# Kernel tuning notes

Hardware: AMD Instinct MI355X
Metric: run time of the kernel (lower is better)

## Reference

```python
import jax, jax.numpy as jnp
import numpy as np

HID, D, NH, NL = 1024, 64, 16, 128  # hidden_dim, head_dim, num_head, num_landmarks


def iterative_inv(mat, n_iter=6):
    # Moore-Penrose pseudo-inverse via Newton-Schulz (Nystromformer), fp32.
    I = jnp.eye(mat.shape[-1], dtype=mat.dtype)
    K = mat
    denom = (jnp.max(jnp.sum(jnp.abs(K), axis=-2), axis=-1)
             * jnp.max(jnp.sum(jnp.abs(K), axis=-1), axis=-1))[..., None, None]
    V = jnp.swapaxes(K, -1, -2) / denom  # Z0 = K^T / (||K||_1 ||K||_inf)
    for _ in range(n_iter):
        KV = K @ V
        V = 0.25 * V @ (13.0 * I - KV @ (15.0 * I - KV @ (7.0 * I - KV)))
    return V


def nystrom_forward(X, mask, Wq, bq, Wk, bk, Wv, bv, Wo, bo):
    B, orig_len, _ = X.shape
    pad_len = NL - orig_len % NL  # always >= 1, matches torch code
    L = orig_len + pad_len
    Xp = jnp.pad(X, ((0, 0), (0, pad_len), (0, 0)))

    def split(Y):  # [B, L, NH*D] -> [B, NH, L, D]
        return Y.reshape(B, L, NH, D).transpose(0, 2, 1, 3)

    Q = split(Xp @ Wq.T + bq).astype(jnp.float32)
    K = split(Xp @ Wk.T + bk).astype(jnp.float32)
    V = split(Xp @ Wv.T + bv).astype(jnp.float32)

    m = mask[:, None, :, None]  # [B,1,L,1]
    scale = 1.0 / (D ** 0.25)   # 1/sqrt(sqrt(head_dim)) applied to both Q and K
    Q = Q * m * scale
    K = K * m * scale

    seg = L // NL
    Q_l = Q.reshape(B, NH, NL, seg, D).mean(axis=-2)  # landmarks via segment means
    K_l = K.reshape(B, NH, NL, seg, D).mean(axis=-2)

    kernel_1 = jax.nn.softmax(jnp.einsum('bhnd,bhld->bhnl', Q, K_l), axis=-1)   # [B,H,L,NL]
    kernel_2 = jax.nn.softmax(jnp.einsum('bhld,bhmd->bhlm', Q_l, K_l), axis=-1)  # [B,H,NL,NL]
    scores_3 = jnp.einsum('bhld,bhnd->bhln', Q_l, K) - 1e9 * (1.0 - mask[:, None, None, :])
    kernel_3 = jax.nn.softmax(scores_3, axis=-1)                                 # [B,H,NL,L]

    out = kernel_1 @ (iterative_inv(kernel_2) @ (kernel_3 @ V))  # [B,H,L,D]
    out = out.transpose(0, 2, 1, 3).reshape(B, L, NH * D)
    out = out @ Wo.T + bo
    return out[:, :orig_len]


def setup_inputs() -> dict:
    key = jax.random.key(0)
    ks = jax.random.split(key, 9)
    B, S = 2, 4095
    Lpad = S + (NL - S % NL)
    s = 0.02
    return {
        'X': jax.random.normal(ks[0], (B, S, HID), dtype=jnp.float32),
        'mask': jnp.ones((B, Lpad), dtype=jnp.float32),
        'Wq': jax.random.normal(ks[1], (NH * D, HID), dtype=jnp.float32) * s,
        'bq': jnp.zeros((NH * D,), dtype=jnp.float32),
        'Wk': jax.random.normal(ks[2], (NH * D, HID), dtype=jnp.float32) * s,
        'bk': jnp.zeros((NH * D,), dtype=jnp.float32),
        'Wv': jax.random.normal(ks[3], (NH * D, HID), dtype=jnp.float32) * s,
        'bv': jnp.zeros((NH * D,), dtype=jnp.float32),
        'Wo': jax.random.normal(ks[4], (HID, NH * D), dtype=jnp.float32) * s,
        'bo': jnp.zeros((HID,), dtype=jnp.float32),
    }


def reference(X, mask, Wq, bq, Wk, bk, Wv, bv, Wo, bo):
    return nystrom_forward(X, mask, Wq, bq, Wk, bk, Wv, bv, Wo, bo)
```

## Files before the change

### kernel.cpp

```cpp
#include <hip/hip_runtime.h>
#include <hip/hip_bf16.h>
#include <math.h>

#define S_ORIG 4095
#define LPAD   4096
#define NHEADS 16
#define DH     64
#define NLM    128
#define BHT    32
#define HIDDEN 1024
#define QKSCALE 0.35355339059327373f

typedef unsigned short u16;
typedef short s16x8 __attribute__((ext_vector_type(8)));
typedef float f32x4 __attribute__((ext_vector_type(4)));

#define IDX64(r, c)  ((r) * 64 + ((c) ^ (((r) & 7) << 3)))
#define IDX128(r, c) ((r) * 128 + ((c) ^ (((r) & 7) << 3)))

__device__ inline void split2(float x, u16& h, u16& l) {
    __hip_bfloat16 bh = __float2bfloat16(x);
    float fh = __bfloat162float(bh);
    __hip_bfloat16 bl = __float2bfloat16(x - fh);
    h = *(u16*)&bh;
    l = *(u16*)&bl;
}

__device__ inline float bf16f(u16 b) {
    unsigned u = ((unsigned)b) << 16;
    return *(float*)&u;
}

__global__ __launch_bounds__(256) void k_split_x(const float* __restrict__ X,
                                                 u16* __restrict__ XH,
                                                 u16* __restrict__ XL) {
    int idx = blockIdx.x * 256 + threadIdx.x;
    int gr = idx >> 8;
    int c4 = (idx & 255) * 4;
    int b = gr >> 12, l = gr & (LPAD - 1);
    float4 v = make_float4(0.f, 0.f, 0.f, 0.f);
    if (l < S_ORIG) v = *(const float4*)(X + ((size_t)b * S_ORIG + l) * HIDDEN + c4);
    ushort4 h4, l4;
    split2(v.x, h4.x, l4.x); split2(v.y, h4.y, l4.y);
    split2(v.z, h4.z, l4.z); split2(v.w, h4.w, l4.w);
    size_t o = (size_t)gr * HIDDEN + c4;
    *(ushort4*)(XH + o) = h4;
    *(ushort4*)(XL + o) = l4;
}

__global__ __launch_bounds__(256) void k_split_w4(
    const float* __restrict__ W0, const float* __restrict__ W1,
    const float* __restrict__ W2, const float* __restrict__ W3,
    u16* __restrict__ H0, u16* __restrict__ L0,
    u16* __restrict__ H1, u16* __restrict__ L1,
    u16* __restrict__ H2, u16* __restrict__ L2,
    u16* __restrict__ H3, u16* __restrict__ L3) {
    int ws = blockIdx.y;
    const float* W = (ws == 0) ? W0 : (ws == 1) ? W1 : (ws == 2) ? W2 : W3;
    u16* H = (ws == 0) ? H0 : (ws == 1) ? H1 : (ws == 2) ? H2 : H3;
    u16* L = (ws == 0) ? L0 : (ws == 1) ? L1 : (ws == 2) ? L2 : L3;
    int idx = blockIdx.x * 256 + threadIdx.x;
    size_t o = (size_t)idx * 4;
    float4 v = *(const float4*)(W + o);
    ushort4 h4, l4;
    split2(v.x, h4.x, l4.x); split2(v.y, h4.y, l4.y);
    split2(v.z, h4.z, l4.z); split2(v.w, h4.w, l4.w);
    *(ushort4*)(H + o) = h4;
    *(ushort4*)(L + o) = l4;
}

__global__ __launch_bounds__(256) void k_gemm_bf16(
    const u16* __restrict__ AH, const u16* __restrict__ AL,
    const u16* __restrict__ B0H, const u16* __restrict__ B0L,
    const u16* __restrict__ B1H, const u16* __restrict__ B1L,
    const u16* __restrict__ B2H, const u16* __restrict__ B2L,
    const float* __restrict__ bias0, const float* __restrict__ bias1,
    const float* __restrict__ bias2, const float* __restrict__ mask,
    u16* __restrict__ QPH, u16* __restrict__ QPL,
    u16* __restrict__ KPH, u16* __restrict__ KPL,
    u16* __restrict__ VPH, u16* __restrict__ VPL,
    float* __restrict__ outF, int mode)
{
    __shared__ u16 Ah_lds[128 * 64];
    __shared__ u16 Al_lds[128 * 64];
    __shared__ u16 Bh_lds[128 * 64];
    __shared__ u16 Bl_lds[128 * 64];
    int tid = threadIdx.x;
    int seg = (mode == 0) ? (blockIdx.y >> 3) : 0;
    int row0 = blockIdx.x * 128;
    int col0 = (mode == 0) ? ((blockIdx.y & 7) * 128) : (blockIdx.y * 128);
    const u16* BH = (seg == 0) ? B0H : (seg == 1) ? B1H : B2H;
    const u16* BL = (seg == 0) ? B0L : (seg == 1) ? B1L : B2L;
    const float* bias = (seg == 0) ? bias0 : (seg == 1) ? bias1 : bias2;
    u16* PH = (seg == 0) ? QPH : (seg == 1) ? KPH : VPH;
    u16* PL = (seg == 0) ? QPL : (seg == 1) ? KPL : VPL;

    int lane = tid & 63, wv = tid >> 6;
    int wr = (wv >> 1) * 64, wc = (wv & 1) * 64;
    int lr = lane & 15, lk = lane >> 4;
    int sr8 = tid >> 3, sc = tid & 7;

    f32x4 acc[4][4] = {};

    for (int kt = 0; kt < 1024; kt += 64) {
        #pragma unroll
        for (int h = 0; h < 4; ++h) {
            int r = sr8 + h * 32;
            int csrc = (sc ^ (r & 7)) * 8;
            size_t ga = (size_t)(row0 + r) * HIDDEN + kt + csrc;
            size_t gb = (size_t)(col0 + r) * HIDDEN + kt + csrc;
            int ldst = r * 64 + sc * 8;
            __builtin_amdgcn_global_load_lds(
                (const __attribute__((address_space(1))) void*)(AH + ga),
                (__attribute__((address_space(3))) void*)(&Ah_lds[ldst]), 16, 0, 0);
            __builtin_amdgcn_global_load_lds(
                (const __attribute__((address_space(1))) void*)(AL + ga),
                (__attribute__((address_space(3))) void*)(&Al_lds[ldst]), 16, 0, 0);
            __builtin_amdgcn_global_load_lds(
                (const __attribute__((address_space(1))) void*)(BH + gb),
                (__attribute__((address_space(3))) void*)(&Bh_lds[ldst]), 16, 0, 0);
            __builtin_amdgcn_global_load_lds(
                (const __attribute__((address_space(1))) void*)(BL + gb),
                (__attribute__((address_space(3))) void*)(&Bl_lds[ldst]), 16, 0, 0);
        }
        __syncthreads();
        #pragma unroll
        for (int kc = 0; kc < 2; ++kc) {
            s16x8 ah[4], al[4], bh4[4], bl4[4];
            #pragma unroll
            for (int i = 0; i < 4; ++i) {
                int ra = wr + i * 16 + lr;
                int rb = wc + i * 16 + lr;
                int ca = (((kc << 2) + lk) ^ (ra & 7)) * 8;
                int cb = (((kc << 2) + lk) ^ (rb & 7)) * 8;
                ah[i]  = *(const s16x8*)&Ah_lds[ra * 64 + ca];
                al[i]  = *(const s16x8*)&Al_lds[ra * 64 + ca];
                bh4[i] = *(const s16x8*)&Bh_lds[rb * 64 + cb];
                bl4[i] = *(const s16x8*)&Bl_lds[rb * 64 + cb];
            }
            #pragma unroll
            for (int i = 0; i < 4; ++i)
                #pragma unroll
                for (int j = 0; j < 4; ++j)
                    acc[i][j] = __builtin_amdgcn_mfma_f32_16x16x32_bf16(ah[i], bh4[j], acc[i][j], 0, 0, 0);
            #pragma unroll
            for (int i = 0; i < 4; ++i)
                #pragma unroll
                for (int j = 0; j < 4; ++j)
                    acc[i][j] = __builtin_amdgcn_mfma_f32_16x16x32_bf16(ah[i], bl4[j], acc[i][j], 0, 0, 0);
            #pragma unroll
            for (int i = 0; i < 4; ++i)
                #pragma unroll
                for (int j = 0; j < 4; ++j)
                    acc[i][j] = __builtin_amdgcn_mfma_f32_16x16x32_bf16(al[i], bh4[j], acc[i][j], 0, 0, 0);
        }
        __syncthreads();
    }

    #pragma unroll
    for (int i = 0; i < 4; ++i) {
        #pragma unroll
        for (int j = 0; j < 4; ++j) {
            int cc = col0 + wc + j * 16 + lr;
            float bval = bias[cc];
            #pragma unroll
            for (int q = 0; q < 4; ++q) {
                int rr = row0 + wr + i * 16 + lk * 4 + q;
                int bb = rr >> 12, l = rr & (LPAD - 1);
                float val = acc[i][j][q] + bval;
                if (mode == 0) {
                    if (seg < 2) val *= mask[(size_t)bb * LPAD + l] * QKSCALE;
                    size_t oi = (((size_t)bb * NHEADS + (cc >> 6)) * LPAD + l) * DH + (cc & 63);
                    u16 hh2, ll2; split2(val, hh2, ll2);
                    PH[oi] = hh2;
                    PL[oi] = ll2;
                } else {
                    if (l < S_ORIG)
                        outF[((size_t)bb * S_ORIG + l) * HIDDEN + cc] = val;
                }
            }
        }
    }
}

__global__ void k_landmarks(const u16* __restrict__ QPH, const u16* __restrict__ QPL,
                            const u16* __restrict__ KPH, const u16* __restrict__ KPL,
                            float* __restrict__ QL, float* __restrict__ KL,
                            u16* __restrict__ QLPH, u16* __restrict__ QLPL) {
    int n = blockIdx.x, bh = blockIdx.y, d = threadIdx.x;
    size_t base = ((size_t)bh * LPAD + n * 32) * DH + d;
    float sq = 0.f, sk = 0.f;
    #pragma unroll
    for (int s = 0; s < 32; ++s) {
        size_t a = base + (size_t)s * DH;
        sq += bf16f(QPH[a]) + bf16f(QPL[a]);
        sk += bf16f(KPH[a]) + bf16f(KPL[a]);
    }
    float ql = sq * (1.f / 32.f), kl = sk * (1.f / 32.f);
    size_t oi = ((size_t)bh * NLM + n) * DH + d;
    QL[oi] = ql;
    KL[oi] = kl;
    u16 hh2, ll2; split2(ql, hh2, ll2);
    QLPH[oi] = hh2;
    QLPL[oi] = ll2;
}

__global__ __launch_bounds__(256) void k_qlk_v0(const float* __restrict__ QLb,
                                                const float* __restrict__ Bsrc,
                                                float* __restrict__ K2out,
                                                float* __restrict__ VA) {
    __shared__ float Qt[64][132];
    __shared__ float Bt[64][132];
    __shared__ float redx[256];
    int tid = threadIdx.x;
    int tx = tid & 15, ty = tid >> 4;
    int bh = blockIdx.y;
    const float* QLp = QLb + (size_t)bh * NLM * DH;
    const float* Bp = Bsrc + (size_t)bh * NLM * DH;

    #pragma unroll
    for (int q = 0; q < 8; ++q) {
        int idx = tid + q * 256;
        int r = idx >> 4, d4 = idx & 15;
        float4 v = *(const float4*)(QLp + (size_t)r * DH + d4 * 4);
        Qt[d4 * 4 + 0][r] = v.x; Qt[d4 * 4 + 1][r] = v.y;
        Qt[d4 * 4 + 2][r] = v.z; Qt[d4 * 4 + 3][r] = v.w;
        float4 w = *(const float4*)(Bp + (size_t)r * DH + d4 * 4);
        Bt[d4 * 4 + 0][r] = w.x; Bt[d4 * 4 + 1][r] = w.y;
        Bt[d4 * 4 + 2][r] = w.z; Bt[d4 * 4 + 3][r] = w.w;
    }
    __syncthreads();

    float acc[8][8];
    #pragma unroll
    for (int i = 0; i < 8; ++i)
        #pragma unroll
        for (int j = 0; j < 8; ++j) acc[i][j] = 0.f;

    #pragma unroll
    for (int k = 0; k < 64; ++k) {
        float av[8], bv[8];
        float4 t0 = *(const float4*)&Qt[k][ty * 4];
        float4 t1 = *(const float4*)&Qt[k][64 + ty * 4];
        float4 t2 = *(const float4*)&Bt[k][tx * 4];
        float4 t3 = *(const float4*)&Bt[k][64 + tx * 4];
        av[0]=t0.x; av[1]=t0.y; av[2]=t0.z; av[3]=t0.w;
        av[4]=t1.x; av[5]=t1.y; av[6]=t1.z; av[7]=t1.w;
        bv[0]=t2.x; bv[1]=t2.y; bv[2]=t2.z; bv[3]=t2.w;
        bv[4]=t3.x; bv[5]=t3.y; bv[6]=t3.z; bv[7]=t3.w;
        #pragma unroll
        for (int i = 0; i < 8; ++i)
            #pragma unroll
            for (int j = 0; j < 8; ++j)
                acc[i][j] = fmaf(av[i], bv[j], acc[i][j]);
    }

    float m[8], s[8];
    #pragma unroll
    for (int i = 0; i < 8; ++i) {
        m[i] = acc[i][0];
        #pragma unroll
        for (int j = 1; j < 8; ++j) m[i] = fmaxf(m[i], acc[i][j]);
    }
    #pragma unroll
    for (int o = 8; o >= 1; o >>= 1)
        #pragma unroll
        for (int i = 0; i < 8; ++i) m[i] = fmaxf(m[i], __shfl_xor(m[i], o));
    #pragma unroll
    for (int i = 0; i < 8; ++i) {
        s[i] = 0.f;
        #pragma unroll
        for (int j = 0; j < 8; ++j) {
            acc[i][j] = expf(acc[i][j] - m[i]);
            s[i] += acc[i][j];
        }
    }
    #pragma unroll
    for (int o = 8; o >= 1; o >>= 1)
        #pragma unroll
        for (int i = 0; i < 8; ++i) s[i] += __shfl_xor(s[i], o);
    #pragma unroll
    for (int i = 0; i < 8; ++i) {
        float inv = 1.f / s[i];
        #pragma unroll
        for (int j = 0; j < 8; ++j) acc[i][j] *= inv;
    }

    #pragma unroll
    for (int i = 0; i < 8; ++i) {
        int r = (i >> 2) * 64 + ty * 4 + (i & 3);
        #pragma unroll
        for (int jh = 0; jh < 2; ++jh) {
            int c = jh * 64 + tx * 4;
            float4 res;
            res.x = acc[i][jh * 4 + 0]; res.y = acc[i][jh * 4 + 1];
            res.z = acc[i][jh * 4 + 2]; res.w = acc[i][jh * 4 + 3];
            *(float4*)(K2out + ((size_t)bh * NLM + r) * NLM + c) = res;
        }
    }

    float rmax = 0.f;
    #pragma unroll
    for (int i = 0; i < 8; ++i) {
        float rs = 0.f;
        #pragma unroll
        for (int j = 0; j < 8; ++j) rs += acc[i][j];
        rs += __shfl_xor(rs, 1);
        rs += __shfl_xor(rs, 2);
        rs += __shfl_xor(rs, 4);
        rs += __shfl_xor(rs, 8);
        rmax = fmaxf(rmax, rs);
    }
    redx[tid] = rmax;
    __syncthreads();
    for (int st = 128; st > 0; st >>= 1) {
        if (tid < st) redx[tid] = fmaxf(redx[tid], redx[tid + st]);
        __syncthreads();
    }
    float rmax_blk = redx[0];
    __syncthreads();

    float* colbuf = &Qt[0][0];
    #pragma unroll
    for (int j = 0; j < 8; ++j) {
        int c = (j >> 2) * 64 + tx * 4 + (j & 3);
        float cp = 0.f;
        #pragma unroll
        for (int i = 0; i < 8; ++i) cp += acc[i][j];
        colbuf[ty * 128 + c] = cp;
    }
    __syncthreads();
    float cs = 0.f;
    if (tid < 128) {
        #pragma unroll
        for (int t2 = 0; t2 < 16; ++t2) cs += colbuf[t2 * 128 + tid];
    }
    redx[tid] = cs;
    __syncthreads();
    for (int st = 128; st > 0; st >>= 1) {
        if (tid < st) redx[tid] = fmaxf(redx[tid], redx[tid + st]);
        __syncthreads();
    }
    float invden = 1.f / (rmax_blk * redx[0]);

    float* VAp = VA + (size_t)bh * NLM * NLM;
    #pragma unroll
    for (int i = 0; i < 8; ++i) {
        int r = (i >> 2) * 64 + ty * 4 + (i & 3);
        #pragma unroll
        for (int j = 0; j < 8; ++j) {
            int c = (j >> 2) * 64 + tx * 4 + (j & 3);
            VAp[(size_t)c * NLM + r] = acc[i][j] * invden;
        }
    }
}

__global__ __launch_bounds__(256) void k_bmm(const float* __restrict__ Ab,
                                             const float* __restrict__ Bb,
                                             float* __restrict__ Cb,
                                             float* __restrict__ C2b,
                                             int N, float alpha, float sI,
                                             float alpha2, float sI2) {
    __shared__ float At[128][36];
    __shared__ float Bs[128][36];
    int tid = threadIdx.x;
    int tx = tid & 15, ty = tid >> 4;
    int bh = blockIdx.z;
    int r0 = blockIdx.y * 32, c0 = blockIdx.x * 32;
    const float* A = Ab + (size_t)bh * NLM * NLM;
    const float* Bm = Bb + (size_t)bh * NLM * N;

    #pragma unroll
    for (int q = 0; q < 4; ++q) {
        int idx = tid + q * 256;
        int r = idx >> 5, k4 = idx & 31;
        float4 v = *(const float4*)(A + (size_t)(r0 + r) * NLM + k4 * 4);
        At[k4 * 4 + 0][r] = v.x; At[k4 * 4 + 1][r] = v.y;
        At[k4 * 4 + 2][r] = v.z; At[k4 * 4 + 3][r] = v.w;
        int bk = idx >> 3, c4 = idx & 7;
        float4 w = *(const float4*)(Bm + (size_t)bk * N + c0 + c4 * 4);
        *(float4*)&Bs[bk][c4 * 4] = w;
    }
    __syncthreads();

    float acc[2][2] = {};
    #pragma unroll 8
    for (int k = 0; k < 128; ++k) {
        float2 a2 = *(const float2*)&At[k][ty * 2];
        float2 b2 = *(const float2*)&Bs[k][tx * 2];
        acc[0][0] = fmaf(a2.x, b2.x, acc[0][0]);
        acc[0][1] = fmaf(a2.x, b2.y, acc[0][1]);
        acc[1][0] = fmaf(a2.y, b2.x, acc[1][0]);
        acc[1][1] = fmaf(a2.y, b2.y, acc[1][1]);
    }

    float* C = Cb + (size_t)bh * NLM * N;
    float* C2 = C2b ? (C2b + (size_t)bh * NLM * N) : nullptr;
    #pragma unroll
    for (int i = 0; i < 2; ++i) {
        int gr = r0 + ty * 2 + i;
        #pragma unroll
        for (int j = 0; j < 2; ++j) {
            int gc = c0 + tx * 2 + j;
            float idadd = (gr == gc) ? 1.f : 0.f;
            C[(size_t)gr * N + gc] = alpha * acc[i][j] + sI * idadd;
            if (C2) C2[(size_t)gr * N + gc] = alpha2 * acc[i][j] + sI2 * idadd;
        }
    }
}

__global__ __launch_bounds__(256) void k_flashk3(const u16* __restrict__ QLPH,
                                                 const u16* __restrict__ QLPL,
                                                 const u16* __restrict__ KPH,
                                                 const u16* __restrict__ KPL,
                                                 const u16* __restrict__ VPH,
                                                 const u16* __restrict__ VPL,
                                                 const float* __restrict__ mask,
                                                 float* __restrict__ PO,
                                                 float* __restrict__ ML) {
    __shared__ u16 lds[32768];
    u16* QLh = lds;
    u16* QLl = lds + 4096;
    u16* Kh  = lds + 8192;
    u16* Kl  = lds + 12288;
    u16* Vth = lds + 16384;
    u16* Vtl = lds + 20480;
    u16* Ph  = lds + 24576;
    u16* Pl  = lds + 28672;

    int tid = threadIdx.x;
    int lane = tid & 63, wv = tid >> 6;
    int lr = lane & 15, lk = lane >> 4;
    int sp = blockIdx.x, qh = blockIdx.y, bh = blockIdx.z;
    int b = bh >> 4;
    int q0 = qh * 64;
    int wr16 = wv * 16;

    #pragma unroll
    for (int q = 0; q < 2; ++q) {
        int idx = tid + q * 256;
        int r = idx >> 3, sc = idx & 7;
        int csrc = (sc ^ (r & 7)) * 8;
        size_t g = ((size_t)bh * NLM + q0 + r) * DH + csrc;
        __builtin_amdgcn_global_load_lds(
            (const __attribute__((address_space(1))) void*)(QLPH + g),
            (__attribute__((address_space(3))) void*)(&QLh[idx * 8]), 16, 0, 0);
        __builtin_amdgcn_global_load_lds(
            (const __attribute__((address_space(1))) void*)(QLPL + g),
            (__attribute__((address_space(3))) void*)(&QLl[idx * 8]), 16, 0, 0);
    }

    float m_run[4] = {-1e30f, -1e30f, -1e30f, -1e30f};
    float l_run[4] = {0.f, 0.f, 0.f, 0.f};
    f32x4 t5[4] = {};

    for (int t = 0; t < 8; ++t) {
        int kt0 = sp * 512 + t * 64;
        #pragma unroll
        for (int q = 0; q < 2; ++q) {
            int idx = tid + q * 256;
            int r = idx >> 3, sc = idx & 7;
            int csrc = (sc ^ (r & 7)) * 8;
            size_t g = ((size_t)bh * LPAD + kt0 + r) * DH + csrc;
            __builtin_amdgcn_global_load_lds(
                (const __attribute__((address_space(1))) void*)(KPH + g),
                (__attribute__((address_space(3))) void*)(&Kh[idx * 8]), 16, 0, 0);
            __builtin_amdgcn_global_load_lds(
                (const __attribute__((address_space(1))) void*)(KPL + g),
                (__attribute__((address_space(3))) void*)(&Kl[idx * 8]), 16, 0, 0);
        }
        #pragma unroll
        for (int q = 0; q < 4; ++q) {
            int idx = tid + q * 256;
            int n = idx & 63, dg = idx >> 6;
            int d4 = dg * 4;
            size_t g = ((size_t)bh * LPAD + kt0 + n) * DH + d4;
            ushort4 h4 = *(const ushort4*)(VPH + g);
            ushort4 l4 = *(const ushort4*)(VPL + g);
            #pragma unroll
            for (int e = 0; e < 4; ++e) {
                Vth[IDX64(d4 + e, n)] = (&h4.x)[e];
                Vtl[IDX64(d4 + e, n)] = (&l4.x)[e];
            }
        }
        __syncthreads();

        f32x4 t4[4] = {};
        #pragma unroll
        for (int tt = 0; tt < 3; ++tt) {
            const u16* Xs = (tt == 2) ? QLl : QLh;
            const u16* Ys = (tt == 1) ? Kl : Kh;
            #pragma unroll
            for (int kc = 0; kc < 2; ++kc) {
                s16x8 a = *(const s16x8*)&Xs[IDX64(wr16 + lr, kc * 32 + lk * 8)];
                s16x8 bfr[4];
                #pragma unroll
                for (int j = 0; j < 4; ++j)
                    bfr[j] = *(const s16x8*)&Ys[IDX64(j * 16 + lr, kc * 32 + lk * 8)];
                #pragma unroll
                for (int j = 0; j < 4; ++j)
                    t4[j] = __builtin_amdgcn_mfma_f32_16x16x32_bf16(a, bfr[j], t4[j], 0, 0, 0);
            }
        }

        #pragma unroll
        for (int j = 0; j < 4; ++j) {
            float pen = 1e9f * (1.f - mask[(size_t)b * LPAD + kt0 + j * 16 + lr]);
            #pragma unroll
            for (int q = 0; q < 4; ++q) t4[j][q] -= pen;
        }

        float alpha[4];
        #pragma unroll
        for (int q = 0; q < 4; ++q) {
            float tm = t4[0][q];
            #pragma unroll
            for (int j = 1; j < 4; ++j) tm = fmaxf(tm, t4[j][q]);
            tm = fmaxf(tm, __shfl_xor(tm, 1));
            tm = fmaxf(tm, __shfl_xor(tm, 2));
            tm = fmaxf(tm, __shfl_xor(tm, 4));
            tm = fmaxf(tm, __shfl_xor(tm, 8));
            float mn = fmaxf(m_run[q], tm);
            float al = expf(m_run[q] - mn);
            float s = 0.f;
            #pragma unroll
            for (int j = 0; j < 4; ++j) {
                t4[j][q] = expf(t4[j][q] - mn);
                s += t4[j][q];
            }
            s += __shfl_xor(s, 1);
            s += __shfl_xor(s, 2);
            s += __shfl_xor(s, 4);
            s += __shfl_xor(s, 8);
            l_run[q] = l_run[q] * al + s;
            m_run[q] = mn;
            alpha[q] = al;
        }
        #pragma unroll
        for (int j = 0; j < 4; ++j)
            #pragma unroll
            for (int q = 0; q < 4; ++q) t5[j][q] *= alpha[q];

        #pragma unroll
        for (int j = 0; j < 4; ++j) {
            int col = j * 16 + lr;
            #pragma unroll
            for (int q = 0; q < 4; ++q) {
                int row = wr16 + lk * 4 + q;
                u16 hh2, ll2; split2(t4[j][q], hh2, ll2);
                Ph[IDX64(row, col)] = hh2;
                Pl[IDX64(row, col)] = ll2;
            }
        }

        #pragma unroll
        for (int tt = 0; tt < 3; ++tt) {
            const u16* Xs = (tt == 2) ? Pl : Ph;
            const u16* Ys = (tt == 1) ? Vtl : Vth;
            #pragma unroll
            for (int kc = 0; kc < 2; ++kc) {
                s16x8 a = *(const s16x8*)&Xs[IDX64(wr16 + lr, kc * 32 + lk * 8)];
                s16x8 bfr[4];
                #pragma unroll
                for (int j = 0; j < 4; ++j)
                    bfr[j] = *(const s16x8*)&Ys[IDX64(j * 16 + lr, kc * 32 + lk * 8)];
                #pragma unroll
                for (int j = 0; j < 4; ++j)
                    t5[j] = __builtin_amdgcn_mfma_f32_16x16x32_bf16(a, bfr[j], t5[j], 0, 0, 0);
            }
        }
        __syncthreads();
    }

    size_t pb = (size_t)(bh * 16 + qh * 8 + sp) * 64;
    #pragma unroll
    for (int j = 0; j < 4; ++j) {
        int d = j * 16 + lr;
        #pragma unroll
        for (int q = 0; q < 4; ++q) {
            int row = wr16 + lk * 4 + q;
            PO[(pb + row) * 64 + d] = t5[j][q];
        }
    }
    if (lr == 0) {
        #pragma unroll
        for (int q = 0; q < 4; ++q) {
            int row = wr16 + lk * 4 + q;
            ML[(pb + row) * 2 + 0] = m_run[q];
            ML[(pb + row) * 2 + 1] = l_run[q];
        }
    }
}

__global__ void k_flash_combine(const float* __restrict__ PO,
                                const float* __restrict__ ML,
                                float* __restrict__ K3V) {
    int idx = blockIdx.x * 256 + threadIdx.x;
    int bh = idx >> 13, rem = idx & 8191;
    int g = rem >> 6, d = rem & 63;
    int qh = g >> 6, rl = g & 63;
    size_t rb = (size_t)(bh * 16 + qh * 8) * 64 + rl;
    float mstar = -1e30f;
    #pragma unroll
    for (int sp = 0; sp < 8; ++sp)
        mstar = fmaxf(mstar, ML[(rb + (size_t)sp * 64) * 2]);
    float osum = 0.f, lsum = 0.f;
    #pragma unroll
    for (int sp = 0; sp < 8; ++sp) {
        size_t r = rb + (size_t)sp * 64;
        float wgt = expf(ML[r * 2] - mstar);
        osum += wgt * PO[r * 64 + d];
        lsum += wgt * ML[r * 2 + 1];
    }
    K3V[idx] = osum / lsum;
}

__global__ __launch_bounds__(256) void k_attn(const u16* __restrict__ QPH,
                                              const u16* __restrict__ QPL,
                                              const float* __restrict__ KLb,
                                              const float* __restrict__ MMb,
                                              u16* __restrict__ ATH,
                                              u16* __restrict__ ATL) {
    __shared__ u16 lds[49152];
    u16* Qh  = lds;
    u16* Ql  = lds + 8192;
    u16* KLh = lds + 16384;
    u16* KLl = lds + 24576;
    u16* Ph  = lds;
    u16* Pl  = lds + 16384;
    u16* Mth = lds + 32768;
    u16* Mtl = lds + 40960;

    int tid = threadIdx.x;
    int lane = tid & 63, wv = tid >> 6;
    int lr = lane & 15, lk = lane >> 4;
    int l0 = blockIdx.x * 128, bh = blockIdx.y;
    int b = bh >> 4, hh = bh & 15;
    int wrA = wv * 32;

    #pragma unroll
    for (int q = 0; q < 4; ++q) {
        int idx = tid + q * 256;
        int r = idx >> 3, sc = idx & 7;
        int csrc = (sc ^ (r & 7)) * 8;
        size_t g = ((size_t)bh * LPAD + l0 + r) * DH + csrc;
        __builtin_amdgcn_global_load_lds(
            (const __attribute__((address_space(1))) void*)(QPH + g),
            (__attribute__((address_space(3))) void*)(&Qh[idx * 8]), 16, 0, 0);
        __builtin_amdgcn_global_load_lds(
            (const __attribute__((address_space(1))) void*)(QPL + g),
            (__attribute__((address_space(3))) void*)(&Ql[idx * 8]), 16, 0, 0);
    }
    #pragma unroll
    for (int q = 0; q < 4; ++q) {
        int idx = tid + q * 256;
        int r = idx >> 3, c8 = (idx & 7) * 8;
        float4 w0 = *(const float4*)(KLb + ((size_t)bh * NLM + r) * DH + c8);
        float4 w1 = *(const float4*)(KLb + ((size_t)bh * NLM + r) * DH + c8 + 4);
        float ys[8] = {w0.x, w0.y, w0.z, w0.w, w1.x, w1.y, w1.z, w1.w};
        s16x8 h8, l8;
        #pragma unroll
        for (int e = 0; e < 8; ++e) {
            u16 hh2, ll2; split2(ys[e], hh2, ll2);
            h8[e] = (short)hh2; l8[e] = (short)ll2;
        }
        *(s16x8*)&KLh[IDX64(r, c8)] = h8;
        *(s16x8*)&KLl[IDX64(r, c8)] = l8;
    }
    #pragma unroll
    for (int q = 0; q < 8; ++q) {
        int idx = tid + q * 256;
        int n = idx >> 4, d4 = (idx & 15) * 4;
        float4 v = *(const float4*)(MMb + ((size_t)bh * NLM + n) * DH + d4);
        float xs[4] = {v.x, v.y, v.z, v.w};
        #pragma unroll
        for (int e = 0; e < 4; ++e) {
            u16 hh2, ll2; split2(xs[e], hh2, ll2);
            Mth[IDX128(d4 + e, n)] = hh2;
            Mtl[IDX128(d4 + e, n)] = ll2;
        }
    }
    __syncthreads();

    f32x4 t4[2][8] = {};
    #pragma unroll
    for (int t = 0; t < 3; ++t) {
        const u16* Xs = (t == 2) ? Ql : Qh;
        const u16* Ys = (t == 1) ? KLl : KLh;
        #pragma unroll
        for (int kc = 0; kc < 2; ++kc) {
            s16x8 a[2], bfr[8];
            #pragma unroll
            for (int i = 0; i < 2; ++i)
                a[i] = *(const s16x8*)&Xs[IDX64(wrA + i * 16 + lr, kc * 32 + lk * 8)];
            #pragma unroll
            for (int j = 0; j < 8; ++j)
                bfr[j] = *(const s16x8*)&Ys[IDX64(j * 16 + lr, kc * 32 + lk * 8)];
            #pragma unroll
            for (int i = 0; i < 2; ++i)
                #pragma unroll
                for (int j = 0; j < 8; ++j)
                    t4[i][j] = __builtin_amdgcn_mfma_f32_16x16x32_bf16(a[i], bfr[j], t4[i][j], 0, 0, 0);
        }
    }

    #pragma unroll
    for (int i = 0; i < 2; ++i)
        #pragma unroll
        for (int q = 0; q < 4; ++q) {
            float m = t4[i][0][q];
            #pragma unroll
            for (int j = 1; j < 8; ++j) m = fmaxf(m, t4[i][j][q]);
            m = fmaxf(m, __shfl_xor(m, 1));
            m = fmaxf(m, __shfl_xor(m, 2));
            m = fmaxf(m, __shfl_xor(m, 4));
            m = fmaxf(m, __shfl_xor(m, 8));
            float s = 0.f;
            #pragma unroll
            for (int j = 0; j < 8; ++j) {
                t4[i][j][q] = expf(t4[i][j][q] - m);
                s += t4[i][j][q];
            }
            s += __shfl_xor(s, 1);
            s += __shfl_xor(s, 2);
            s += __shfl_xor(s, 4);
            s += __shfl_xor(s, 8);
            float inv = 1.f / s;
            #pragma unroll
            for (int j = 0; j < 8; ++j) t4[i][j][q] *= inv;
        }

    __syncthreads();
    #pragma unroll
    for (int i = 0; i < 2; ++i)
        #pragma unroll
        for (int j = 0; j < 8; ++j) {
            int col = j * 16 + lr;
            #pragma unroll
            for (int q = 0; q < 4; ++q) {
                int row = wrA + i * 16 + lk * 4 + q;
                u16 hh2, ll2; split2(t4[i][j][q], hh2, ll2);
                Ph[IDX128(row, col)] = hh2;
                Pl[IDX128(row, col)] = ll2;
            }
        }
    __syncthreads();

    f32x4 t5[2][4] = {};
    #pragma unroll
    for (int t = 0; t < 3; ++t) {
        const u16* Xs = (t == 2) ? Pl : Ph;
        const u16* Ys = (t == 1) ? Mtl : Mth;
        #pragma unroll
        for (int kc = 0; kc < 4; ++kc) {
            s16x8 a[2], bfr[4];
            #pragma unroll
            for (int i = 0; i < 2; ++i)
                a[i] = *(const s16x8*)&Xs[IDX128(wrA + i * 16 + lr, kc * 32 + lk * 8)];
            #pragma unroll
            for (int j = 0; j < 4; ++j)
                bfr[j] = *(const s16x8*)&Ys[IDX128(j * 16 + lr, kc * 32 + lk * 8)];
            #pragma unroll
            for (int i = 0; i < 2; ++i)
                #pragma unroll
                for (int j = 0; j < 4; ++j)
                    t5[i][j] = __builtin_amdgcn_mfma_f32_16x16x32_bf16(a[i], bfr[j], t5[i][j], 0, 0, 0);
        }
    }

    #pragma unroll
    for (int i = 0; i < 2; ++i)
        #pragma unroll
        for (int j = 0; j < 4; ++j) {
            int d = j * 16 + lr;
            #pragma unroll
            for (int q = 0; q < 4; ++q) {
                int l = l0 + wrA + i * 16 + lk * 4 + q;
                size_t base = ((size_t)b * LPAD + l) * HIDDEN + hh * DH + d;
                u16 hh2, ll2; split2(t5[i][j][q], hh2, ll2);
                ATH[base] = hh2;
                ATL[base] = ll2;
            }
        }
}

extern "C" void kernel_launch(void* const* d_in, const int* in_sizes, int n_in,
                              void* d_out, int out_size, void* d_ws, size_t ws_size,
                              hipStream_t stream) {
    (void)in_sizes; (void)n_in; (void)out_size; (void)ws_size;
    const float* X    = (const float*)d_in[0];
    const float* mask = (const float*)d_in[1];
    const float* Wq   = (const float*)d_in[2];
    const float* bq   = (const float*)d_in[3];
    const float* Wk   = (const float*)d_in[4];
    const float* bk   = (const float*)d_in[5];
    const float* Wv   = (const float*)d_in[6];
    const float* bv   = (const float*)d_in[7];
    const float* Wo   = (const float*)d_in[8];
    const float* bo   = (const float*)d_in[9];
    float* out = (float*)d_out;
    float* w = (float*)d_ws;

    size_t o = 0;
    u16* WQH = (u16*)(w + o); o += (size_t)HIDDEN * HIDDEN / 2;
    u16* WQL = (u16*)(w + o); o += (size_t)HIDDEN * HIDDEN / 2;
    u16* WKH = (u16*)(w + o); o += (size_t)HIDDEN * HIDDEN / 2;
    u16* WKL = (u16*)(w + o); o += (size_t)HIDDEN * HIDDEN / 2;
    u16* WVH = (u16*)(w + o); o += (size_t)HIDDEN * HIDDEN / 2;
    u16* WVL = (u16*)(w + o); o += (size_t)HIDDEN * HIDDEN / 2;
    u16* WOH = (u16*)(w + o); o += (size_t)HIDDEN * HIDDEN / 2;
    u16* WOL = (u16*)(w + o); o += (size_t)HIDDEN * HIDDEN / 2;
    float* Q   = w + o; o += (size_t)BHT * LPAD * DH;
    float* K   = w + o; o += (size_t)BHT * LPAD * DH;
    float* V   = w + o; o += (size_t)BHT * LPAD * DH;
    float* QL  = w + o; o += (size_t)BHT * NLM * DH;
    float* KL  = w + o; o += (size_t)BHT * NLM * DH;
    float* K2  = w + o; o += (size_t)BHT * NLM * NLM;
    float* VA  = w + o; o += (size_t)BHT * NLM * NLM;
    float* VB  = w + o; o += (size_t)BHT * NLM * NLM;
    float* KV  = w + o; o += (size_t)BHT * NLM * NLM;
    float* P1  = w + o; o += (size_t)BHT * NLM * NLM;
    float* T3  = w + o; o += (size_t)BHT * NLM * NLM;
    float* PK  = w + o; o += (size_t)BHT * 16 * NLM * DH;
    float* K3V = w + o; o += (size_t)BHT * NLM * DH;
    float* MM  = w + o; o += (size_t)BHT * NLM * DH;
    float* SC  = w + o; o += (size_t)BHT * NLM * LPAD;

    u16* QPH = (u16*)Q;
    u16* QPL = QPH + (size_t)BHT * LPAD * DH;
    u16* KPH = (u16*)K;
    u16* KPL = KPH + (size_t)BHT * LPAD * DH;
    u16* VPH = (u16*)V;
    u16* VPL = VPH + (size_t)BHT * LPAD * DH;

    float* PO = PK;
    float* ML = PK + (size_t)BHT * 16 * 64 * 64;

    u16* XH  = (u16*)SC;
    u16* XL  = XH + (size_t)2 * LPAD * HIDDEN;
    u16* ATH = (u16*)SC;
    u16* ATL = ATH + (size_t)2 * LPAD * HIDDEN;
    u16* QLPH = (u16*)SC + (size_t)32 * 1024 * 1024;
    u16* QLPL = QLPH + (size_t)BHT * NLM * DH;

    k_split_x<<<8192, 256, 0, stream>>>(X, XH, XL);
    k_split_w4<<<dim3(1024, 4), 256, 0, stream>>>(Wq, Wk, Wv, Wo,
        WQH, WQL, WKH, WKL, WVH, WVL, WOH, WOL);

    k_gemm_bf16<<<dim3(64, 24), 256, 0, stream>>>(
        XH, XL, WQH, WQL, WKH, WKL, WVH, WVL, bq, bk, bv, mask,
        QPH, QPL, KPH, KPL, VPH, VPL, nullptr, 0);

    k_landmarks<<<dim3(NLM, BHT), 64, 0, stream>>>(QPH, QPL, KPH, KPL, QL, KL, QLPH, QLPL);

    k_qlk_v0<<<dim3(1, BHT), 256, 0, stream>>>(QL, KL, K2, VA);

    k_flashk3<<<dim3(8, 2, BHT), 256, 0, stream>>>(QLPH, QLPL, KPH, KPL, VPH, VPL, mask, PO, ML);
    k_flash_combine<<<(BHT * NLM * DH) / 256, 256, 0, stream>>>(PO, ML, K3V);

    float* cur = VA;
    float* nxt = VB;
    for (int it = 0; it < 6; ++it) {
        k_bmm<<<dim3(4, 4, BHT), 256, 0, stream>>>(K2, cur, KV, P1, NLM, 1.f, 0.f, -1.f, 7.f);
        k_bmm<<<dim3(4, 4, BHT), 256, 0, stream>>>(KV, P1, T3, nullptr, NLM, -1.f, 15.f, 0.f, 0.f);
        k_bmm<<<dim3(4, 4, BHT), 256, 0, stream>>>(KV, T3, P1, nullptr, NLM, -1.f, 13.f, 0.f, 0.f);
        k_bmm<<<dim3(4, 4, BHT), 256, 0, stream>>>(cur, P1, nxt, nullptr, NLM, 0.25f, 0.f, 0.f, 0.f);
        float* t = cur; cur = nxt; nxt = t;
    }

    k_bmm<<<dim3(2, 4, BHT), 256, 0, stream>>>(cur, K3V, MM, nullptr, DH, 1.f, 0.f, 0.f, 0.f);

    k_attn<<<dim3(32, BHT), 256, 0, stream>>>(QPH, QPL, KL, MM, ATH, ATL);

    k_gemm_bf16<<<dim3(64, 8), 256, 0, stream>>>(
        ATH, ATL, WOH, WOL, nullptr, nullptr, nullptr, nullptr, bo, nullptr,
        nullptr, nullptr, nullptr, nullptr, nullptr, nullptr, nullptr, nullptr, out, 1);
}
```

Baseline: 541.1 us.

## Fuse Newton-Schulz iteration bmm launches into one cooperative kernel with grid syncs

Replaces the 25 separate small batched-matmul launches of the pseudo-inverse iteration and final product with a single cooperative kernel. Grid-wide syncs separate the dependent matmul steps. The aim is to remove per-launch overhead and idle gaps between tiny kernels. In exchange, every block must be co-resident (512 blocks of 256 threads), and each grid.sync has its own cost.

```diff
diff --git a/kernel.cpp b/kernel.cpp
--- a/kernel.cpp
+++ b/kernel.cpp
@@ -1,6 +1,9 @@
 #include <hip/hip_runtime.h>
 #include <hip/hip_bf16.h>
+#include <hip/hip_cooperative_groups.h>
 #include <math.h>
+
+namespace cg = cooperative_groups;
 
 #define S_ORIG 4095
 #define LPAD   4096
@@ -355,20 +358,16 @@
     }
 }
 
-__global__ __launch_bounds__(256) void k_bmm(const float* __restrict__ Ab,
-                                             const float* __restrict__ Bb,
-                                             float* __restrict__ Cb,
-                                             float* __restrict__ C2b,
-                                             int N, float alpha, float sI,
-                                             float alpha2, float sI2) {
-    __shared__ float At[128][36];
-    __shared__ float Bs[128][36];
-    int tid = threadIdx.x;
-    int tx = tid & 15, ty = tid >> 4;
-    int bh = blockIdx.z;
-    int r0 = blockIdx.y * 32, c0 = blockIdx.x * 32;
+__device__ __forceinline__ void bmm_step(
+    const float* __restrict__ Ab, const float* __restrict__ Bb,
+    float* __restrict__ Cb, float* __restrict__ C2b,
+    int N, float alpha, float sI, float alpha2, float sI2,
+    int bh, int r0, int c0, int tid,
+    float (*At)[36], float (*Bs)[36])
+{
     const float* A = Ab + (size_t)bh * NLM * NLM;
     const float* Bm = Bb + (size_t)bh * NLM * N;
+    int tx = tid & 15, ty = tid >> 4;
 
     #pragma unroll
     for (int q = 0; q < 4; ++q) {
@@ -407,6 +406,36 @@
             if (C2) C2[(size_t)gr * N + gc] = alpha2 * acc[i][j] + sI2 * idadd;
         }
     }
+}
+
+__global__ __launch_bounds__(256) void k_newton_coop(
+    const float* __restrict__ K2, float* __restrict__ VA, float* __restrict__ VB,
+    float* __restrict__ KV, float* __restrict__ P1, float* __restrict__ T3,
+    const float* __restrict__ K3V, float* __restrict__ MM)
+{
+    __shared__ float At[128][36];
+    __shared__ float Bs[128][36];
+    cg::grid_group grid = cg::this_grid();
+
+    int tid = threadIdx.x;
+    int bh = blockIdx.z;
+    int r0 = blockIdx.y * 32, c0 = blockIdx.x * 32;
+
+    float* cur = VA;
+    float* nxt = VB;
+    for (int it = 0; it < 6; ++it) {
+        bmm_step(K2, cur, KV, P1, NLM, 1.f, 0.f, -1.f, 7.f, bh, r0, c0, tid, At, Bs);
+        grid.sync();
+        bmm_step(KV, P1, T3, nullptr, NLM, -1.f, 15.f, 0.f, 0.f, bh, r0, c0, tid, At, Bs);
+        grid.sync();
+        bmm_step(KV, T3, P1, nullptr, NLM, -1.f, 13.f, 0.f, 0.f, bh, r0, c0, tid, At, Bs);
+        grid.sync();
+        bmm_step(cur, P1, nxt, nullptr, NLM, 0.25f, 0.f, 0.f, 0.f, bh, r0, c0, tid, At, Bs);
+        grid.sync();
+        float* t = cur; cur = nxt; nxt = t;
+    }
+    if (c0 < DH)
+        bmm_step(cur, K3V, MM, nullptr, DH, 1.f, 0.f, 0.f, 0.f, bh, r0, c0, tid, At, Bs);
 }
 
 __global__ __launch_bounds__(256) void k_flashk3(const u16* __restrict__ QLPH,
@@ -858,17 +887,14 @@
     k_flashk3<<<dim3(8, 2, BHT), 256, 0, stream>>>(QLPH, QLPL, KPH, KPL, VPH, VPL, mask, PO, ML);
     k_flash_combine<<<(BHT * NLM * DH) / 256, 256, 0, stream>>>(PO, ML, K3V);
 
-    float* cur = VA;
-    float* nxt = VB;
-    for (int it = 0; it < 6; ++it) {
-        k_bmm<<<dim3(4, 4, BHT), 256, 0, stream>>>(K2, cur, KV, P1, NLM, 1.f, 0.f, -1.f, 7.f);
-        k_bmm<<<dim3(4, 4, BHT), 256, 0, stream>>>(KV, P1, T3, nullptr, NLM, -1.f, 15.f, 0.f, 0.f);
-        k_bmm<<<dim3(4, 4, BHT), 256, 0, stream>>>(KV, T3, P1, nullptr, NLM, -1.f, 13.f, 0.f, 0.f);
-        k_bmm<<<dim3(4, 4, BHT), 256, 0, stream>>>(cur, P1, nxt, nullptr, NLM, 0.25f, 0.f, 0.f, 0.f);
-        float* t = cur; cur = nxt; nxt = t;
-    }
-
-    k_bmm<<<dim3(2, 4, BHT), 256, 0, stream>>>(cur, K3V, MM, nullptr, DH, 1.f, 0.f, 0.f, 0.f);
+    {
+        const float* K2c = K2;
+        const float* K3Vc = K3V;
+        void* args[] = { (void*)&K2c, (void*)&VA, (void*)&VB, (void*)&KV,
+                         (void*)&P1, (void*)&T3, (void*)&K3Vc, (void*)&MM };
+        hipLaunchCooperativeKernel((void*)k_newton_coop, dim3(4, 4, BHT),
+                                   dim3(256), args, 0, stream);
+    }
 
     k_attn<<<dim3(32, BHT), 256, 0, stream>>>(QPH, QPL, KL, MM, ATH, ATL);
 
```

Result: slower. 1.962 ms (+262.7%).
